# Performance work log

Hardware: AMD Instinct MI355X
Metric: run time of the kernel (lower is better)

Reference implementation:

```python
import jax, jax.numpy as jnp
import numpy as np

IN_FEATURES = 4096
OUT_FEATURES = 768
N_BITS = 8
SCALE = float(2 ** N_BITS - 1)  # 255
REG_WEIGHT = 0.001


def setup_inputs() -> dict:
    key = jax.random.key(0)
    k1, k2, k3 = jax.random.split(key, 3)
    latent = jax.random.normal(k1, (1024, IN_FEATURES), dtype=jnp.float32)
    true_sum = jax.random.uniform(k2, (1024, OUT_FEATURES * N_BITS), dtype=jnp.float32)
    # nn.init.uniform_(weight, -0.1, 0.1)
    weight = jax.random.uniform(k3, (IN_FEATURES, OUT_FEATURES * N_BITS),
                                dtype=jnp.float32, minval=-0.1, maxval=0.1)
    return {"latent": latent, "true_sum": true_sum, "weight": weight}


def _powers():
    # [1, 2, 4, ..., 2^(n-1)] with the top (sign) bit negated -> two's complement
    p = 2.0 ** jnp.arange(N_BITS, dtype=jnp.float32)
    return p.at[-1].multiply(-1.0)


def reference(latent, true_sum, weight):
    prob_weights = jax.nn.sigmoid(weight)                      # [in, out*n_bits]
    # min(|p-0|, |p-1|) = min(p, 1-p) for p in (0,1)
    reg_loss = REG_WEIGHT * jnp.minimum(prob_weights, 1.0 - prob_weights).mean()

    powers = _powers()                                         # [n_bits]
    int_weights = jnp.einsum('iob,b->io',
                             prob_weights.reshape(IN_FEATURES, -1, N_BITS),
                             powers)                           # [in, out]
    int_sum = jnp.einsum('nob,b->no',
                         true_sum.reshape(true_sum.shape[0], -1, N_BITS),
                         powers)                               # [B, out]

    # (latent[:, :, None] * int_weights[None]).sum(-2) == latent @ int_weights
    pred = jnp.einsum('bi,io->bo', latent, int_weights)        # [B, out]

    recon_loss = jnp.mean((pred / SCALE - int_sum / SCALE) ** 2)
    return (recon_loss + reg_loss, recon_loss, reg_loss)
```

## Files before the change

### kernel.cpp

```cpp
#include <hip/hip_runtime.h>
#include <hip/hip_bf16.h>
#include <stdint.h>

#define IN_F   4096
#define OUT_F  768
#define OUTB   (OUT_F * 8)
#define BATCH  1024
#define SPLITK 4
#define KSPAN  (IN_F / SPLITK)
#define NIT    (KSPAN / 32)
#define PLANE  (BATCH * OUT_F)

typedef short short8  __attribute__((ext_vector_type(8)));
typedef float f32x4   __attribute__((ext_vector_type(4)));
typedef unsigned int u32;

__device__ __forceinline__ ushort f2bf(float f) {
    uint32_t u = __builtin_bit_cast(uint32_t, f);
    u += 0x7FFFu + ((u >> 16) & 1u);
    return (ushort)(u >> 16);
}

__device__ __forceinline__ float waveReduceSum(float v) {
    #pragma unroll
    for (int off = 32; off > 0; off >>= 1) v += __shfl_down(v, off, 64);
    return v;
}

__device__ __forceinline__ void glds16(const void* g, void* l) {
    __builtin_amdgcn_global_load_lds(
        (const __attribute__((address_space(1))) u32*)g,
        (__attribute__((address_space(3))) u32*)l, 16, 0, 0);
}

#define WS_WP    12582912
#define WS_LABF  18874368
#define WS_REGP  27262976
#define WS_SQP   27269120

__global__ __launch_bounds__(256) void k_weights(const float* __restrict__ w,
                                                 const float* __restrict__ latent,
                                                 ushort* __restrict__ wp,
                                                 ushort* __restrict__ labf,
                                                 float* __restrict__ regpart) {
    if (blockIdx.x >= 1536) {
        int t = (blockIdx.x - 1536) * 256 + threadIdx.x;
        const float4* src = (const float4*)latent;
        uint4* dst = (uint4*)labf;
        #pragma unroll
        for (int j = 0; j < 4; j++) {
            int o = j * 131072 + t;
            float4 a0 = src[2 * o];
            float4 a1 = src[2 * o + 1];
            union { ushort u[8]; uint4 v; } pk;
            pk.u[0] = f2bf(a0.x); pk.u[1] = f2bf(a0.y); pk.u[2] = f2bf(a0.z); pk.u[3] = f2bf(a0.w);
            pk.u[4] = f2bf(a1.x); pk.u[5] = f2bf(a1.y); pk.u[6] = f2bf(a1.z); pk.u[7] = f2bf(a1.w);
            dst[o] = pk.v;
        }
        return;
    }

    int t  = blockIdx.x * 256 + threadIdx.x;
    int o  = t % OUT_F;
    int i8 = t / OUT_F;
    const float* src = w + (size_t)(i8 * 8) * OUTB + (size_t)o * 8;

    const float P[8] = {1.f, 2.f, 4.f, 8.f, 16.f, 32.f, 64.f, -128.f};
    float regsum = 0.f;
    union { ushort u[8]; uint4 v; } pk;

    #pragma unroll
    for (int r = 0; r < 8; r++) {
        float4 a = *(const float4*)(src + (size_t)r * OUTB);
        float4 b = *(const float4*)(src + (size_t)r * OUTB + 4);
        float x[8] = {a.x, a.y, a.z, a.w, b.x, b.y, b.z, b.w};
        float iw = 0.f;
        #pragma unroll
        for (int j = 0; j < 8; j++) {
            float p = __builtin_amdgcn_rcpf(1.f + __expf(-x[j]));
            iw += p * P[j];
            regsum += fminf(p, 1.f - p);
        }
        pk.u[r] = f2bf(iw);
    }
    *(uint4*)(wp + ((size_t)i8 * OUT_F + o) * 8) = pk.v;

    float ws = waveReduceSum(regsum);
    __shared__ float red[4];
    int lane = threadIdx.x & 63, wv = threadIdx.x >> 6;
    if (lane == 0) red[wv] = ws;
    __syncthreads();
    if (threadIdx.x == 0) regpart[blockIdx.x] = red[0] + red[1] + red[2] + red[3];
}

__global__ __launch_bounds__(256) void k_gemm(const ushort* __restrict__ labf,
                                              const ushort* __restrict__ wp,
                                              float* __restrict__ predp) {
    __shared__ __align__(16) ushort lA[2][64 * 40];
    __shared__ __align__(16) ushort lB[2][4 * 1032];

    const int tid  = threadIdx.x;
    const int n0   = blockIdx.x * 64;
    const int m0   = blockIdx.y * 64;
    const int kbase = blockIdx.z * KSPAN;
    const int lane = tid & 63, w = tid >> 6;
    const int wm = w >> 1, wn = w & 1;
    const int quad = lane >> 4, l16 = lane & 15;

    f32x4 acc[2][2] = {{{0.f,0.f,0.f,0.f},{0.f,0.f,0.f,0.f}},
                       {{0.f,0.f,0.f,0.f},{0.f,0.f,0.f,0.f}}};

    const int ar = tid >> 2, ac = tid & 3;
    const ushort* aptr = labf + (size_t)(m0 + ar) * IN_F + kbase + ac * 8;
    const ushort* bptr = wp + ((size_t)(kbase / 8 + w) * OUT_F + n0 + lane) * 8;

    int buf = 0;
    glds16(bptr, &lB[0][w * 1032]);
    uint4 aR = *(const uint4*)aptr;
    *(uint4*)&lA[0][ar * 40 + ac * 8] = aR;
    __syncthreads();

    for (int it = 0; it < NIT; ++it) {
        const int nxt = buf ^ 1;
        if (it + 1 < NIT) {
            glds16(bptr + (size_t)(it + 1) * 4 * OUT_F * 8, &lB[nxt][w * 1032]);
            aR = *(const uint4*)(aptr + (it + 1) * 32);
        }
        short8 af0 = *(short8*)&lA[buf][(wm * 32 + l16) * 40 + quad * 8];
        short8 af1 = *(short8*)&lA[buf][(wm * 32 + 16 + l16) * 40 + quad * 8];
        short8 bf0 = *(short8*)&lB[buf][quad * 1032 + (wn * 32 + l16) * 8];
        short8 bf1 = *(short8*)&lB[buf][quad * 1032 + (wn * 32 + 16 + l16) * 8];
        acc[0][0] = __builtin_amdgcn_mfma_f32_16x16x32_bf16(af0, bf0, acc[0][0], 0, 0, 0);
        acc[0][1] = __builtin_amdgcn_mfma_f32_16x16x32_bf16(af0, bf1, acc[0][1], 0, 0, 0);
        acc[1][0] = __builtin_amdgcn_mfma_f32_16x16x32_bf16(af1, bf0, acc[1][0], 0, 0, 0);
        acc[1][1] = __builtin_amdgcn_mfma_f32_16x16x32_bf16(af1, bf1, acc[1][1], 0, 0, 0);
        if (it + 1 < NIT) *(uint4*)&lA[nxt][ar * 40 + ac * 8] = aR;
        __syncthreads();
        buf = nxt;
    }

    float* plane = predp + (size_t)blockIdx.z * PLANE;
    #pragma unroll
    for (int fm = 0; fm < 2; fm++)
    #pragma unroll
    for (int fn = 0; fn < 2; fn++)
    #pragma unroll
    for (int r = 0; r < 4; r++) {
        int m = m0 + wm * 32 + fm * 16 + quad * 4 + r;
        int n = n0 + wn * 32 + fn * 16 + l16;
        plane[(size_t)m * OUT_F + n] = acc[fm][fn][r];
    }
}

__global__ __launch_bounds__(256) void k_epi(const float* __restrict__ predp,
                                             const float* __restrict__ tsum,
                                             float* __restrict__ sqpart) {
    int n = blockIdx.x * 256 + threadIdx.x;
    int m = blockIdx.y;
    size_t idx = (size_t)m * OUT_F + n;
    float p = predp[idx] + predp[idx + PLANE] + predp[idx + 2 * PLANE] + predp[idx + 3 * PLANE];
    const float* ts = tsum + (size_t)m * OUTB + (size_t)n * 8;
    float4 t0 = *(const float4*)ts;
    float4 t1 = *(const float4*)(ts + 4);
    float isum = t0.x + 2.f * t0.y + 4.f * t0.z + 8.f * t0.w
               + 16.f * t1.x + 32.f * t1.y + 64.f * t1.z - 128.f * t1.w;
    float d = p - isum;
    float lsum = d * d;

    float wsum = waveReduceSum(lsum);
    __shared__ float red[4];
    if ((threadIdx.x & 63) == 0) red[threadIdx.x >> 6] = wsum;
    __syncthreads();
    if (threadIdx.x == 0)
        sqpart[blockIdx.y * 3 + blockIdx.x] = red[0] + red[1] + red[2] + red[3];
}

__global__ __launch_bounds__(256) void k_fin(const float* __restrict__ regpart,
                                             const float* __restrict__ sqpart,
                                             float* __restrict__ out) {
    int tid = threadIdx.x;
    float r = 0.f, s = 0.f;
    #pragma unroll
    for (int j = 0; j < 6; j++) r += regpart[tid + j * 256];
    #pragma unroll
    for (int j = 0; j < 12; j++) s += sqpart[tid + j * 256];
    r = waveReduceSum(r);
    s = waveReduceSum(s);
    __shared__ float redR[4], redS[4];
    int lane = tid & 63, wv = tid >> 6;
    if (lane == 0) { redR[wv] = r; redS[wv] = s; }
    __syncthreads();
    if (tid == 0) {
        float R = redR[0] + redR[1] + redR[2] + redR[3];
        float S = redS[0] + redS[1] + redS[2] + redS[3];
        float recon = S / ((float)(BATCH * OUT_F) * 255.f * 255.f);
        float reg   = 0.001f * R / (float)((size_t)IN_F * OUTB);
        out[0] = recon + reg;
        out[1] = recon;
        out[2] = reg;
    }
}

extern "C" void kernel_launch(void* const* d_in, const int* in_sizes, int n_in,
                              void* d_out, int out_size, void* d_ws, size_t ws_size,
                              hipStream_t stream) {
    const float* latent = (const float*)d_in[0];
    const float* tsum   = (const float*)d_in[1];
    const float* weight = (const float*)d_in[2];
    float* out     = (float*)d_out;
    float* predp   = (float*)d_ws;
    ushort* wp     = (ushort*)((char*)d_ws + WS_WP);
    ushort* labf   = (ushort*)((char*)d_ws + WS_LABF);
    float* regpart = (float*)((char*)d_ws + WS_REGP);
    float* sqpart  = (float*)((char*)d_ws + WS_SQP);

    k_weights<<<2048, 256, 0, stream>>>(weight, latent, wp, labf, regpart);
    k_gemm<<<dim3(OUT_F / 64, BATCH / 64, SPLITK), 256, 0, stream>>>(labf, wp, predp);
    k_epi<<<dim3(3, BATCH), 256, 0, stream>>>(predp, tsum, sqpart);
    k_fin<<<1, 256, 0, stream>>>(regpart, sqpart, out);
}
```

Baseline: 204.5 us.

## Fuse split-K reduction, loss epilogue and final reduction into GEMM via atomic tile counters

The GEMM kernel now uses a K-tile of 64 instead of 32, so there are half as many main-loop iterations and barriers per block. Per-tile atomic counters let the last split-K block of each output tile sum the four partial planes, compute the squared error against true_sum, and write a per-tile partial. A global done-counter then lets the final block compute the three loss outputs. This removes two kernel launches and their gaps, but adds threadfence and atomic overhead, a serialized tail in the last blocks, and larger LDS use per block.

```diff
diff --git a/kernel.cpp b/kernel.cpp
--- a/kernel.cpp
+++ b/kernel.cpp
@@ -8,12 +8,20 @@
 #define BATCH  1024
 #define SPLITK 4
 #define KSPAN  (IN_F / SPLITK)
-#define NIT    (KSPAN / 32)
+#define BK     64
+#define NIT    (KSPAN / BK)
 #define PLANE  (BATCH * OUT_F)
+#define NTILE  192
 
 typedef short short8  __attribute__((ext_vector_type(8)));
 typedef float f32x4   __attribute__((ext_vector_type(4)));
 typedef unsigned int u32;
+
+#define WS_WP    12582912
+#define WS_LABF  18874368
+#define WS_REGP  27262976
+#define WS_SQP   27269120
+#define WS_CNT   27269888
 
 __device__ __forceinline__ ushort f2bf(float f) {
     uint32_t u = __builtin_bit_cast(uint32_t, f);
@@ -33,16 +41,14 @@
         (__attribute__((address_space(3))) u32*)l, 16, 0, 0);
 }
 
-#define WS_WP    12582912
-#define WS_LABF  18874368
-#define WS_REGP  27262976
-#define WS_SQP   27269120
-
 __global__ __launch_bounds__(256) void k_weights(const float* __restrict__ w,
                                                  const float* __restrict__ latent,
                                                  ushort* __restrict__ wp,
                                                  ushort* __restrict__ labf,
-                                                 float* __restrict__ regpart) {
+                                                 float* __restrict__ regpart,
+                                                 int* __restrict__ cnt) {
+    if (blockIdx.x == 0 && threadIdx.x < 200) cnt[threadIdx.x] = 0;
+
     if (blockIdx.x >= 1536) {
         int t = (blockIdx.x - 1536) * 256 + threadIdx.x;
         const float4* src = (const float4*)latent;
@@ -95,14 +101,22 @@
 
 __global__ __launch_bounds__(256) void k_gemm(const ushort* __restrict__ labf,
                                               const ushort* __restrict__ wp,
-                                              float* __restrict__ predp) {
-    __shared__ __align__(16) ushort lA[2][64 * 40];
-    __shared__ __align__(16) ushort lB[2][4 * 1032];
+                                              const float* __restrict__ tsum,
+                                              float* __restrict__ predp,
+                                              const float* __restrict__ regpart,
+                                              float* __restrict__ sqpart,
+                                              int* __restrict__ tileCnt,
+                                              int* __restrict__ tilesDone,
+                                              float* __restrict__ out) {
+    __shared__ __align__(16) ushort lA[2][64 * 72];
+    __shared__ __align__(16) ushort lB[2][8 * 1032];
 
     const int tid  = threadIdx.x;
     const int n0   = blockIdx.x * 64;
     const int m0   = blockIdx.y * 64;
-    const int kbase = blockIdx.z * KSPAN;
+    const int bz   = blockIdx.z;
+    const int kbase = bz * KSPAN;
+    const int kg0   = kbase >> 3;
     const int lane = tid & 63, w = tid >> 6;
     const int wm = w >> 1, wn = w & 1;
     const int quad = lane >> 4, l16 = lane & 15;
@@ -111,35 +125,50 @@
                        {{0.f,0.f,0.f,0.f},{0.f,0.f,0.f,0.f}}};
 
     const int ar = tid >> 2, ac = tid & 3;
-    const ushort* aptr = labf + (size_t)(m0 + ar) * IN_F + kbase + ac * 8;
-    const ushort* bptr = wp + ((size_t)(kbase / 8 + w) * OUT_F + n0 + lane) * 8;
+    const ushort* aptr = labf + (size_t)(m0 + ar) * IN_F + kbase + ac * 16;
+    const ushort* bbase = wp + ((size_t)kg0 * OUT_F + n0 + lane) * 8;
 
     int buf = 0;
-    glds16(bptr, &lB[0][w * 1032]);
-    uint4 aR = *(const uint4*)aptr;
-    *(uint4*)&lA[0][ar * 40 + ac * 8] = aR;
+    glds16(bbase + (size_t)(2 * w) * OUT_F * 8,     &lB[0][(2 * w) * 1032]);
+    glds16(bbase + (size_t)(2 * w + 1) * OUT_F * 8, &lB[0][(2 * w + 1) * 1032]);
+    {
+        uint4 a0 = *(const uint4*)aptr;
+        uint4 a1 = *(const uint4*)(aptr + 8);
+        *(uint4*)&lA[0][ar * 72 + ac * 16]     = a0;
+        *(uint4*)&lA[0][ar * 72 + ac * 16 + 8] = a1;
+    }
     __syncthreads();
 
     for (int it = 0; it < NIT; ++it) {
         const int nxt = buf ^ 1;
+        uint4 a0, a1;
         if (it + 1 < NIT) {
-            glds16(bptr + (size_t)(it + 1) * 4 * OUT_F * 8, &lB[nxt][w * 1032]);
-            aR = *(const uint4*)(aptr + (it + 1) * 32);
-        }
-        short8 af0 = *(short8*)&lA[buf][(wm * 32 + l16) * 40 + quad * 8];
-        short8 af1 = *(short8*)&lA[buf][(wm * 32 + 16 + l16) * 40 + quad * 8];
-        short8 bf0 = *(short8*)&lB[buf][quad * 1032 + (wn * 32 + l16) * 8];
-        short8 bf1 = *(short8*)&lB[buf][quad * 1032 + (wn * 32 + 16 + l16) * 8];
-        acc[0][0] = __builtin_amdgcn_mfma_f32_16x16x32_bf16(af0, bf0, acc[0][0], 0, 0, 0);
-        acc[0][1] = __builtin_amdgcn_mfma_f32_16x16x32_bf16(af0, bf1, acc[0][1], 0, 0, 0);
-        acc[1][0] = __builtin_amdgcn_mfma_f32_16x16x32_bf16(af1, bf0, acc[1][0], 0, 0, 0);
-        acc[1][1] = __builtin_amdgcn_mfma_f32_16x16x32_bf16(af1, bf1, acc[1][1], 0, 0, 0);
-        if (it + 1 < NIT) *(uint4*)&lA[nxt][ar * 40 + ac * 8] = aR;
+            const ushort* bp = bbase + (size_t)(it + 1) * 8 * OUT_F * 8;
+            glds16(bp + (size_t)(2 * w) * OUT_F * 8,     &lB[nxt][(2 * w) * 1032]);
+            glds16(bp + (size_t)(2 * w + 1) * OUT_F * 8, &lB[nxt][(2 * w + 1) * 1032]);
+            a0 = *(const uint4*)(aptr + (it + 1) * BK);
+            a1 = *(const uint4*)(aptr + (it + 1) * BK + 8);
+        }
+        #pragma unroll
+        for (int s = 0; s < 2; ++s) {
+            short8 af0 = *(short8*)&lA[buf][(wm * 32 + l16) * 72 + s * 32 + quad * 8];
+            short8 af1 = *(short8*)&lA[buf][(wm * 32 + 16 + l16) * 72 + s * 32 + quad * 8];
+            short8 bf0 = *(short8*)&lB[buf][(s * 4 + quad) * 1032 + (wn * 32 + l16) * 8];
+            short8 bf1 = *(short8*)&lB[buf][(s * 4 + quad) * 1032 + (wn * 32 + 16 + l16) * 8];
+            acc[0][0] = __builtin_amdgcn_mfma_f32_16x16x32_bf16(af0, bf0, acc[0][0], 0, 0, 0);
+            acc[0][1] = __builtin_amdgcn_mfma_f32_16x16x32_bf16(af0, bf1, acc[0][1], 0, 0, 0);
+            acc[1][0] = __builtin_amdgcn_mfma_f32_16x16x32_bf16(af1, bf0, acc[1][0], 0, 0, 0);
+            acc[1][1] = __builtin_amdgcn_mfma_f32_16x16x32_bf16(af1, bf1, acc[1][1], 0, 0, 0);
+        }
+        if (it + 1 < NIT) {
+            *(uint4*)&lA[nxt][ar * 72 + ac * 16]     = a0;
+            *(uint4*)&lA[nxt][ar * 72 + ac * 16 + 8] = a1;
+        }
         __syncthreads();
         buf = nxt;
     }
 
-    float* plane = predp + (size_t)blockIdx.z * PLANE;
+    float* plane = predp + (size_t)bz * PLANE;
     #pragma unroll
     for (int fm = 0; fm < 2; fm++)
     #pragma unroll
@@ -150,49 +179,58 @@
         int n = n0 + wn * 32 + fn * 16 + l16;
         plane[(size_t)m * OUT_F + n] = acc[fm][fn][r];
     }
-}
-
-__global__ __launch_bounds__(256) void k_epi(const float* __restrict__ predp,
-                                             const float* __restrict__ tsum,
-                                             float* __restrict__ sqpart) {
-    int n = blockIdx.x * 256 + threadIdx.x;
-    int m = blockIdx.y;
-    size_t idx = (size_t)m * OUT_F + n;
-    float p = predp[idx] + predp[idx + PLANE] + predp[idx + 2 * PLANE] + predp[idx + 3 * PLANE];
-    const float* ts = tsum + (size_t)m * OUTB + (size_t)n * 8;
-    float4 t0 = *(const float4*)ts;
-    float4 t1 = *(const float4*)(ts + 4);
-    float isum = t0.x + 2.f * t0.y + 4.f * t0.z + 8.f * t0.w
-               + 16.f * t1.x + 32.f * t1.y + 64.f * t1.z - 128.f * t1.w;
-    float d = p - isum;
-    float lsum = d * d;
-
+
+    __threadfence();
+    const int tileIdx = blockIdx.y * 12 + blockIdx.x;
+    __shared__ int sdone;
+    if (tid == 0) sdone = atomicAdd(&tileCnt[tileIdx], 1);
+    __syncthreads();
+    if (sdone != SPLITK - 1) return;
+
+    __threadfence();
+    const int nl = tid & 63;
+    const int mg = tid >> 6;
+    float lsum = 0.f;
+    #pragma unroll 4
+    for (int r = 0; r < 16; ++r) {
+        int m = m0 + mg * 16 + r;
+        int n = n0 + nl;
+        size_t idx = (size_t)m * OUT_F + n;
+        float p = predp[idx] + predp[idx + PLANE] + predp[idx + 2 * PLANE] + predp[idx + 3 * PLANE];
+        const float* ts = tsum + (size_t)m * OUTB + (size_t)n * 8;
+        float4 t0 = *(const float4*)ts;
+        float4 t1 = *(const float4*)(ts + 4);
+        float isum = t0.x + 2.f * t0.y + 4.f * t0.z + 8.f * t0.w
+                   + 16.f * t1.x + 32.f * t1.y + 64.f * t1.z - 128.f * t1.w;
+        float d = p - isum;
+        lsum += d * d;
+    }
     float wsum = waveReduceSum(lsum);
-    __shared__ float red[4];
-    if ((threadIdx.x & 63) == 0) red[threadIdx.x >> 6] = wsum;
-    __syncthreads();
-    if (threadIdx.x == 0)
-        sqpart[blockIdx.y * 3 + blockIdx.x] = red[0] + red[1] + red[2] + red[3];
-}
-
-__global__ __launch_bounds__(256) void k_fin(const float* __restrict__ regpart,
-                                             const float* __restrict__ sqpart,
-                                             float* __restrict__ out) {
-    int tid = threadIdx.x;
-    float r = 0.f, s = 0.f;
-    #pragma unroll
-    for (int j = 0; j < 6; j++) r += regpart[tid + j * 256];
-    #pragma unroll
-    for (int j = 0; j < 12; j++) s += sqpart[tid + j * 256];
+    __shared__ float redS[4];
+    if ((tid & 63) == 0) redS[tid >> 6] = wsum;
+    __syncthreads();
+    __shared__ int sfin;
+    if (tid == 0) {
+        sqpart[tileIdx] = redS[0] + redS[1] + redS[2] + redS[3];
+        __threadfence();
+        sfin = (atomicAdd(tilesDone, 1) == NTILE - 1);
+    }
+    __syncthreads();
+    if (!sfin) return;
+
+    __threadfence();
+    float r = 0.f;
+    #pragma unroll
+    for (int j = 0; j < 6; ++j) r += regpart[tid + j * 256];
+    float s = (tid < NTILE) ? sqpart[tid] : 0.f;
     r = waveReduceSum(r);
     s = waveReduceSum(s);
-    __shared__ float redR[4], redS[4];
-    int lane = tid & 63, wv = tid >> 6;
-    if (lane == 0) { redR[wv] = r; redS[wv] = s; }
+    __shared__ float redR2[4], redS2[4];
+    if ((tid & 63) == 0) { redR2[tid >> 6] = r; redS2[tid >> 6] = s; }
     __syncthreads();
     if (tid == 0) {
-        float R = redR[0] + redR[1] + redR[2] + redR[3];
-        float S = redS[0] + redS[1] + redS[2] + redS[3];
+        float R = redR2[0] + redR2[1] + redR2[2] + redR2[3];
+        float S = redS2[0] + redS2[1] + redS2[2] + redS2[3];
         float recon = S / ((float)(BATCH * OUT_F) * 255.f * 255.f);
         float reg   = 0.001f * R / (float)((size_t)IN_F * OUTB);
         out[0] = recon + reg;
@@ -207,15 +245,15 @@
     const float* latent = (const float*)d_in[0];
     const float* tsum   = (const float*)d_in[1];
     const float* weight = (const float*)d_in[2];
-    float* out     = (float*)d_out;
-    float* predp   = (float*)d_ws;
-    ushort* wp     = (ushort*)((char*)d_ws + WS_WP);
-    ushort* labf   = (ushort*)((char*)d_ws + WS_LABF);
-    float* regpart = (float*)((char*)d_ws + WS_REGP);
-    float* sqpart  = (float*)((char*)d_ws + WS_SQP);
-
-    k_weights<<<2048, 256, 0, stream>>>(weight, latent, wp, labf, regpart);
-    k_gemm<<<dim3(OUT_F / 64, BATCH / 64, SPLITK), 256, 0, stream>>>(labf, wp, predp);
-    k_epi<<<dim3(3, BATCH), 256, 0, stream>>>(predp, tsum, sqpart);
-    k_fin<<<1, 256, 0, stream>>>(regpart, sqpart, out);
-}
+    float* out      = (float*)d_out;
+    float* predp    = (float*)d_ws;
+    ushort* wp      = (ushort*)((char*)d_ws + WS_WP);
+    ushort* labf    = (ushort*)((char*)d_ws + WS_LABF);
+    float* regpart  = (float*)((char*)d_ws + WS_REGP);
+    float* sqpart   = (float*)((char*)d_ws + WS_SQP);
+    int*   cnt      = (int*)((char*)d_ws + WS_CNT);
+
+    k_weights<<<2048, 256, 0, stream>>>(weight, latent, wp, labf, regpart, cnt);
+    k_gemm<<<dim3(OUT_F / 64, BATCH / 64, SPLITK), 256, 0, stream>>>(
+        labf, wp, tsum, predp, regpart, sqpart, cnt, cnt + NTILE, out);
+}
```

New measurement: 322.2 us. +57.5%, slower.
